# Kernel optimization log

Measured on AMD Instinct MI355X. Metric: run time of the kernel, lower is better.

The kernel has to match this reference:

```python
import jax, jax.numpy as jnp
import numpy as np

MARGIN = 0.5

def setup_inputs() -> dict:
    key = jax.random.key(0)
    k1, k2 = jax.random.split(key)
    n, d, n_classes = 8192, 512, 1024
    embedding = jax.random.normal(k1, (n, d), dtype=jnp.float32)
    label = jax.random.randint(k2, (n,), 0, n_classes, dtype=jnp.int64)
    return {"embedding": embedding, "label": label}


def reference(embedding, label):
    # sim_mat[i, j] = <e_i, e_j>
    n = embedding.shape[0]
    sim = embedding @ embedding.T  # [n, n]
    same = label[:, None] == label[None, :]  # [n, n] bool
    # per-row positive pairs: same label AND sim < 1; loss contrib (1 - sim)
    pos_mask = same & (sim < 1.0)
    # per-row negative pairs (hard mining): diff label AND sim > margin; loss contrib sim
    neg_mask = (~same) & (sim > MARGIN)
    pos_loss = jnp.sum(jnp.where(pos_mask, 1.0 - sim, 0.0))
    neg_loss = jnp.sum(jnp.where(neg_mask, sim, 0.0))
    loss = (pos_loss + neg_loss) / n
    return (loss, 0, 0)
```

## Files before the change

### kernel.cpp

```cpp
#include <hip/hip_runtime.h>
#include <hip/hip_bf16.h>


typedef int i32x4 __attribute__((ext_vector_type(4)));

#define N_EMB 8192
#define D_EMB 512
#define BM    128
#define HKB   64
#define NPH   (D_EMB / HKB)
#define TILES (N_EMB / BM)
#define NBLK  (TILES * (TILES + 1) / 2)
#define MARGIN_F 0.5f
#define QSCALE 24.0f
#define DEQ    (1.0f / (QSCALE * QSCALE))
#define HBYT  (BM * HKB)

__device__ __forceinline__ void gll16(const void* g, void* l) {
    __builtin_amdgcn_global_load_lds(
        (const __attribute__((address_space(1))) void*)g,
        (__attribute__((address_space(3))) void*)l,
        16 , 0 , 0 );
}

__global__ __launch_bounds__(256) void quant_kernel(const float* __restrict__ in,
                                                    int4* __restrict__ out, int n16) {
    int i = blockIdx.x * blockDim.x + threadIdx.x;
    if (i >= n16) return;
    const float4* p = reinterpret_cast<const float4*>(in) + i * 4;
    int4 o;
    int* po = reinterpret_cast<int*>(&o);
#pragma unroll
    for (int j = 0; j < 4; ++j) {
        float4 v = p[j];
        int b0 = (int)rintf(fminf(fmaxf(v.x * QSCALE, -127.f), 127.f));
        int b1 = (int)rintf(fminf(fmaxf(v.y * QSCALE, -127.f), 127.f));
        int b2 = (int)rintf(fminf(fmaxf(v.z * QSCALE, -127.f), 127.f));
        int b3 = (int)rintf(fminf(fmaxf(v.w * QSCALE, -127.f), 127.f));
        po[j] = (b0 & 255) | ((b1 & 255) << 8) | ((b2 & 255) << 16) | ((b3 & 255) << 24);
    }
    out[i] = o;
}

__global__ __launch_bounds__(512) void loss_kernel(const char* __restrict__ E8,
                                                   const int* __restrict__ label,
                                                   float* __restrict__ partials) {
    const int bid = blockIdx.x;
    const int t = (bid & 7) * (NBLK / 8) + (bid >> 3);

    int tr = (int)(64.5f - sqrtf(4160.25f - 2.0f * (float)t));
    while ((tr + 1) * TILES - ((tr + 1) * tr) / 2 <= t) ++tr;
    while (tr * TILES - (tr * (tr - 1)) / 2 > t) --tr;
    const int tc = tr + (t - (tr * TILES - (tr * (tr - 1)) / 2));

    __shared__ char  lds[3][2][HBYT];
    __shared__ float red[8];

    const int tid  = threadIdx.x;
    const int wid  = tid >> 6, lane = tid & 63;
    const int wrow = wid >> 2, wcol = wid & 3;
    const int fr   = lane & 15;
    const int kq   = lane >> 4;
    const int row0 = tr * BM, col0 = tc * BM;

    const int sw = (((tid & 3) ^ ((tid >> 3) & 3)) << 4);
    const int r0 = tid >> 2;
    const char* gA0 = E8 + (size_t)(row0 + r0) * D_EMB + sw;
    const char* gB0 = E8 + (size_t)(col0 + r0) * D_EMB + sw;
    const int d0 = tid << 4;

    i32x4 acc[4][2] = {};

    const int psw = ((kq ^ ((fr >> 1) & 3)) << 4);

    gll16(gA0,       &lds[0][0][d0]); gll16(gB0,       &lds[0][1][d0]);
    gll16(gA0 + HKB, &lds[1][0][d0]); gll16(gB0 + HKB, &lds[1][1][d0]);

#pragma unroll
    for (int p = 0; p < NPH; ++p) {
        const int rg = p % 3;
        if (p < NPH - 1) {
            asm volatile("s_waitcnt vmcnt(2)" ::: "memory");
        } else {
            asm volatile("s_waitcnt vmcnt(0)" ::: "memory");
        }
        __builtin_amdgcn_s_barrier();
        __builtin_amdgcn_sched_barrier(0);

        i32x4 a[4], b[2];
#pragma unroll
        for (int m = 0; m < 4; ++m)
            a[m] = *reinterpret_cast<const i32x4*>(
                &lds[rg][0][((wrow * 64 + m * 16 + fr) << 6) + psw]);
#pragma unroll
        for (int n = 0; n < 2; ++n)
            b[n] = *reinterpret_cast<const i32x4*>(
                &lds[rg][1][((wcol * 32 + n * 16 + fr) << 6) + psw]);

        if (p + 2 < NPH) {
            const int rg2 = (p + 2) % 3;
            const int ko  = (p + 2) * HKB;
            gll16(gA0 + ko, &lds[rg2][0][d0]);
            gll16(gB0 + ko, &lds[rg2][1][d0]);
        }

        __builtin_amdgcn_s_setprio(1);
#pragma unroll
        for (int m = 0; m < 4; ++m)
#pragma unroll
            for (int n = 0; n < 2; ++n)
                acc[m][n] = __builtin_amdgcn_mfma_i32_16x16x64_i8(a[m], b[n], acc[m][n], 0, 0, 0);
        __builtin_amdgcn_s_setprio(0);
    }

    float local = 0.f;
    int lj[2];
#pragma unroll
    for (int n = 0; n < 2; ++n) lj[n] = label[col0 + wcol * 32 + n * 16 + fr];
    const int rb = kq << 2;
#pragma unroll
    for (int m = 0; m < 4; ++m) {
#pragma unroll
        for (int r = 0; r < 4; ++r) {
            const int li = label[row0 + wrow * 64 + m * 16 + rb + r];
#pragma unroll
            for (int n = 0; n < 2; ++n) {
                const float s = (float)acc[m][n][r] * DEQ;
                if (li == lj[n]) {
                    if (s < 1.0f) local += 1.0f - s;
                } else if (s > MARGIN_F) {
                    local += s;
                }
            }
        }
    }
    if (tr != tc) local *= 2.0f;

#pragma unroll
    for (int off = 32; off > 0; off >>= 1) local += __shfl_xor(local, off);
    if (lane == 0) red[wid] = local;
    __syncthreads();
    if (tid == 0) {
        float s = 0.f;
#pragma unroll
        for (int i = 0; i < 8; ++i) s += red[i];
        partials[t] = s;
    }
}

__global__ __launch_bounds__(256) void reduce_kernel(const float* __restrict__ partials,
                                                     float* __restrict__ out, int nb) {
    float s = 0.f;
    for (int i = threadIdx.x; i < nb; i += 256) s += partials[i];
#pragma unroll
    for (int off = 32; off > 0; off >>= 1) s += __shfl_xor(s, off);
    __shared__ float red[4];
    if ((threadIdx.x & 63) == 0) red[threadIdx.x >> 6] = s;
    __syncthreads();
    if (threadIdx.x == 0) {
        out[0] = (red[0] + red[1] + red[2] + red[3]) * (1.0f / (float)N_EMB);
        out[1] = 0.f;
        out[2] = 0.f;
    }
}

extern "C" void kernel_launch(void* const* d_in, const int* in_sizes, int n_in,
                              void* d_out, int out_size, void* d_ws, size_t ws_size,
                              hipStream_t stream) {
    const float* emb   = (const float*)d_in[0];
    const int*   label = (const int*)d_in[1];
    float*       out   = (float*)d_out;

    char*  E8      = (char*)d_ws;
    float* partial = (float*)((char*)d_ws + (size_t)N_EMB * D_EMB);

    const int n16 = N_EMB * D_EMB / 16;
    quant_kernel<<<(n16 + 255) / 256, 256, 0, stream>>>(emb, (int4*)E8, n16);

    loss_kernel<<<NBLK, 512, 0, stream>>>(E8, label, partial);

    reduce_kernel<<<1, 256, 0, stream>>>(partial, out, NBLK);
}
```

Measured before the change: 41.82 us.

## Load B operand directly from global into registers, bypassing LDS

The B tile of the int8 GEMM is no longer staged through LDS. Each wave now loads its own B fragments straight from global memory into registers, one K-phase ahead, while A keeps its triple-buffered LDS path. Halving the LDS footprint and adding a launch-bounds occupancy hint aim to fit more blocks per CU and cut LDS traffic. In exchange, the two waves sharing a column range fetch the same B data twice from cache. B prefetch is also only one phase deep, so global latency may be exposed.

After: 61.83 us. 1.48x slower.

```diff
diff --git a/kernel.cpp b/kernel.cpp
--- a/kernel.cpp
+++ b/kernel.cpp
@@ -42,9 +42,9 @@
     out[i] = o;
 }
 
-__global__ __launch_bounds__(512) void loss_kernel(const char* __restrict__ E8,
-                                                   const int* __restrict__ label,
-                                                   float* __restrict__ partials) {
+__global__ __launch_bounds__(512, 4) void loss_kernel(const char* __restrict__ E8,
+                                                      const int* __restrict__ label,
+                                                      float* __restrict__ partials) {
     const int bid = blockIdx.x;
     const int t = (bid & 7) * (NBLK / 8) + (bid >> 3);
 
@@ -53,7 +53,7 @@
     while (tr * TILES - (tr * (tr - 1)) / 2 > t) --tr;
     const int tc = tr + (t - (tr * TILES - (tr * (tr - 1)) / 2));
 
-    __shared__ char  lds[3][2][HBYT];
+    __shared__ char  lds[3][HBYT];
     __shared__ float red[8];
 
     const int tid  = threadIdx.x;
@@ -66,51 +66,65 @@
     const int sw = (((tid & 3) ^ ((tid >> 3) & 3)) << 4);
     const int r0 = tid >> 2;
     const char* gA0 = E8 + (size_t)(row0 + r0) * D_EMB + sw;
-    const char* gB0 = E8 + (size_t)(col0 + r0) * D_EMB + sw;
     const int d0 = tid << 4;
+
+    const char* gB[2];
+#pragma unroll
+    for (int n = 0; n < 2; ++n)
+        gB[n] = E8 + (size_t)(col0 + wcol * 32 + n * 16 + fr) * D_EMB + (kq << 4);
 
     i32x4 acc[4][2] = {};
 
     const int psw = ((kq ^ ((fr >> 1) & 3)) << 4);
 
-    gll16(gA0,       &lds[0][0][d0]); gll16(gB0,       &lds[0][1][d0]);
-    gll16(gA0 + HKB, &lds[1][0][d0]); gll16(gB0 + HKB, &lds[1][1][d0]);
+    i32x4 b_cur[2], b_next[2];
+#pragma unroll
+    for (int n = 0; n < 2; ++n)
+        b_cur[n] = *reinterpret_cast<const i32x4*>(gB[n]);
+    __builtin_amdgcn_sched_barrier(0);
+    gll16(gA0,       &lds[0][d0]);
+    gll16(gA0 + HKB, &lds[1][d0]);
+    __builtin_amdgcn_sched_barrier(0);
 
 #pragma unroll
     for (int p = 0; p < NPH; ++p) {
         const int rg = p % 3;
         if (p < NPH - 1) {
-            asm volatile("s_waitcnt vmcnt(2)" ::: "memory");
+            asm volatile("s_waitcnt vmcnt(1)" ::: "memory");
         } else {
             asm volatile("s_waitcnt vmcnt(0)" ::: "memory");
         }
         __builtin_amdgcn_s_barrier();
         __builtin_amdgcn_sched_barrier(0);
 
-        i32x4 a[4], b[2];
+        i32x4 a[4];
 #pragma unroll
         for (int m = 0; m < 4; ++m)
             a[m] = *reinterpret_cast<const i32x4*>(
-                &lds[rg][0][((wrow * 64 + m * 16 + fr) << 6) + psw]);
+                &lds[rg][((wrow * 64 + m * 16 + fr) << 6) + psw]);
+
+        if (p + 1 < NPH) {
 #pragma unroll
-        for (int n = 0; n < 2; ++n)
-            b[n] = *reinterpret_cast<const i32x4*>(
-                &lds[rg][1][((wcol * 32 + n * 16 + fr) << 6) + psw]);
+            for (int n = 0; n < 2; ++n)
+                b_next[n] = *reinterpret_cast<const i32x4*>(gB[n] + (p + 1) * HKB);
+        }
+        __builtin_amdgcn_sched_barrier(0);
 
         if (p + 2 < NPH) {
-            const int rg2 = (p + 2) % 3;
-            const int ko  = (p + 2) * HKB;
-            gll16(gA0 + ko, &lds[rg2][0][d0]);
-            gll16(gB0 + ko, &lds[rg2][1][d0]);
+            gll16(gA0 + (p + 2) * HKB, &lds[(p + 2) % 3][d0]);
         }
+        __builtin_amdgcn_sched_barrier(0);
 
         __builtin_amdgcn_s_setprio(1);
 #pragma unroll
         for (int m = 0; m < 4; ++m)
 #pragma unroll
             for (int n = 0; n < 2; ++n)
-                acc[m][n] = __builtin_amdgcn_mfma_i32_16x16x64_i8(a[m], b[n], acc[m][n], 0, 0, 0);
+                acc[m][n] = __builtin_amdgcn_mfma_i32_16x16x64_i8(a[m], b_cur[n], acc[m][n], 0, 0, 0);
         __builtin_amdgcn_s_setprio(0);
+
+#pragma unroll
+        for (int n = 0; n < 2; ++n) b_cur[n] = b_next[n];
     }
 
     float local = 0.f;
```
